# Kernel optimization log

Measured on AMD Instinct MI355X. Metric: run time of the kernel, lower is better.

## Reference

```python
import jax, jax.numpy as jnp
import numpy as np
import math

N, D = 4096, 1024


def setup_inputs() -> dict:
    key = jax.random.key(0)
    ks = jax.random.split(key, 8)
    vecs = jax.random.normal(ks[0], (N, D), dtype=jnp.float32)
    mass = jax.random.uniform(ks[1], (N,), dtype=jnp.float32)            # semantic mass in [0,1)
    hops = jax.random.uniform(ks[2], (N,), dtype=jnp.float32) * 5.0      # hop distances in [0,5)
    alive = jax.random.randint(ks[3], (N,), 0, 10) > 0
    is_photon = jax.random.randint(ks[4], (N,), 0, 10) == 0
    W_res_w = jax.random.normal(ks[5], (D, D), dtype=jnp.float32) / np.sqrt(D)
    W_res_b = jnp.zeros((D,), dtype=jnp.float32)
    w_conf_i = jax.random.normal(ks[6], (D,), dtype=jnp.float32) / np.sqrt(2 * D)
    w_conf_j = jax.random.normal(ks[7], (D,), dtype=jnp.float32) / np.sqrt(2 * D)
    b_conf = jnp.zeros((), dtype=jnp.float32)
    log_c = jnp.asarray(math.log(50.0), dtype=jnp.float32)  # 'relationship' domain
    log_G = jnp.zeros((), dtype=jnp.float32)
    return dict(vecs=vecs, mass=mass, hops=hops, alive=alive, is_photon=is_photon,
                W_res_w=W_res_w, W_res_b=W_res_b, w_conf_i=w_conf_i, w_conf_j=w_conf_j,
                b_conf=b_conf, log_c=log_c, log_G=log_G)


def reference(vecs, mass, hops, alive, is_photon, W_res_w, W_res_b,
              w_conf_i, w_conf_j, b_conf, log_c, log_G):
    n = vecs.shape[0]
    c = jnp.maximum(jnp.exp(log_c), 1e-6)
    G = jnp.exp(log_G)

    # Per-row quantities (phi() reads hops/photon from entity i).
    d_light = hops / c                                                   # [N]
    lam = jnp.where(is_photon, 1.0, jnp.exp(-d_light))                   # redshift, [N]
    r2 = jnp.maximum(d_light, 0.1) ** 2                                  # r_safe^2, [N]
    causal_decay = jnp.where(d_light <= 1.0, 1.0, jnp.exp(-d_light + 1.0))  # [N]

    # Causal mask: j must be strictly in the past (j < i).
    idx = jnp.arange(n)
    past = (idx[None, :] < idx[:, None]).astype(vecs.dtype)              # [N,N]
    C = past * causal_decay[:, None]

    # Gravity: G * m_i * m_j / r_i^2
    grav = G * (mass / r2)[:, None] * mass[None, :]                      # [N,N]

    # Resonance: cosine similarity of W_res projections (torch eps=1e-8 norm clamp).
    v = vecs @ W_res_w.T + W_res_b                                       # [N,D]
    vn = v / jnp.maximum(jnp.linalg.norm(v, axis=-1, keepdims=True), 1e-8)
    R = vn @ vn.T                                                        # [N,N]
    zero_norm = jnp.linalg.norm(vecs, axis=-1) < 1e-8                    # [N]
    R = jnp.where(zero_norm[:, None] | zero_norm[None, :], 0.0, R)

    # Conflict gate: sigmoid(W_conflict @ concat(v_i, v_j) + b) = sigmoid(s_i + s_j + b).
    s_i = vecs @ w_conf_i                                                # [N]
    s_j = vecs @ w_conf_j                                                # [N]
    conflict = jax.nn.sigmoid(s_i[:, None] + s_j[None, :] + b_conf)      # [N,N]

    phi_attract = lam[:, None] * grav * C * (0.5 + 0.5 * R)
    phi_repulse = -lam[:, None] * conflict * mass[:, None] * mass[None, :]
    phi = jnp.where(conflict > 0.8, phi_repulse, phi_attract)

    # Black holes and the diagonal produce zero field.
    gate = alive[:, None] & alive[None, :]
    phi = jnp.where(gate & (idx[:, None] != idx[None, :]), phi, 0.0)
    return phi
```

## Files before the change

### kernel.cpp

```cpp
#include <hip/hip_runtime.h>
#include <hip/hip_bf16.h>
#include <math.h>

#define NROW 4096
#define DIM  1024

typedef short v8s __attribute__((ext_vector_type(8)));
typedef float v4f __attribute__((ext_vector_type(4)));

__device__ __forceinline__ ushort f2bf(float f) {
    __hip_bfloat16 h = __float2bfloat16(f);
    union { __hip_bfloat16 h; ushort u; } x; x.h = h; return x.u;
}

__global__ __launch_bounds__(256) void k_rowstats(
    const float* __restrict__ vecs, const float* __restrict__ mass,
    const float* __restrict__ hops, const int* __restrict__ alive,
    const int* __restrict__ is_photon, const float* __restrict__ wci,
    const float* __restrict__ wcj, const float* __restrict__ logc,
    const float* __restrict__ logG, const float* __restrict__ bconf,
    double* __restrict__ s_i, double* __restrict__ s_j,
    float* __restrict__ rowAtt, float* __restrict__ rowRep,
    float* __restrict__ massF, int* __restrict__ flags)
{
    const int row = blockIdx.x, t = threadIdx.x;
    const float* vr = vecs + (size_t)row * DIM;
    const int base = t * 4;
    float4 pv = *(const float4*)&vr[base];
    float4 pi = *(const float4*)&wci[base];
    float4 pj = *(const float4*)&wcj[base];
    double di = (double)pv.x * pi.x + (double)pv.y * pi.y + (double)pv.z * pi.z + (double)pv.w * pi.w;
    double dj = (double)pv.x * pj.x + (double)pv.y * pj.y + (double)pv.z * pj.z + (double)pv.w * pj.w;
    double ss = (double)pv.x * pv.x + (double)pv.y * pv.y + (double)pv.z * pv.z + (double)pv.w * pv.w;
    #pragma unroll
    for (int off = 32; off > 0; off >>= 1) {
        di += __shfl_down(di, off);
        dj += __shfl_down(dj, off);
        ss += __shfl_down(ss, off);
    }
    __shared__ double rd[3][4];
    const int wid = t >> 6;
    if ((t & 63) == 0) { rd[0][wid] = di; rd[1][wid] = dj; rd[2][wid] = ss; }
    __syncthreads();
    if (t == 0) {
        di = rd[0][0] + rd[0][1] + rd[0][2] + rd[0][3];
        dj = rd[1][0] + rd[1][1] + rd[1][2] + rd[1][3];
        ss = rd[2][0] + rd[2][1] + rd[2][2] + rd[2][3];
        double c  = fmax(exp((double)logc[0]), 1e-6);
        double G  = exp((double)logG[0]);
        double dl = (double)hops[row] / c;
        double lam = (is_photon[row] != 0) ? 1.0 : exp(-dl);
        double rs  = fmax(dl, 0.1);
        double cd  = (dl <= 1.0) ? 1.0 : exp(-dl + 1.0);
        double m   = (double)mass[row];
        s_i[row] = di;
        s_j[row] = dj + (double)bconf[0];
        rowAtt[row] = (float)(lam * G * m / (rs * rs) * cd);
        rowRep[row] = (float)(-lam * m);
        massF[row]  = (float)m;
        flags[row]  = ((alive[row] != 0) ? 1 : 0) | ((sqrt(ss) < 1e-8) ? 2 : 0);
    }
}

__global__ __launch_bounds__(256) void k_proj(
    const float* __restrict__ A, const float* __restrict__ B,
    const float* __restrict__ bias, ushort* __restrict__ vout)
{
    __shared__ ushort As[128 * 32], Bs[128 * 32];
    const int t = threadIdx.x;
    const int m0 = blockIdx.y * 128, n0 = blockIdx.x * 128;
    const int wid = t >> 6, lane = t & 63;
    const int wm = wid >> 1, wn = wid & 1;
    const int quad = lane >> 4, l16 = lane & 15;
    v4f acc[4][4];
    #pragma unroll
    for (int i = 0; i < 4; i++)
        #pragma unroll
        for (int j = 0; j < 4; j++) acc[i][j] = (v4f){0.f, 0.f, 0.f, 0.f};

    for (int k0 = 0; k0 < DIM; k0 += 32) {
        #pragma unroll
        for (int p = 0; p < 4; ++p) {
            int c = p * 256 + t;
            int r = c >> 3, co = (c & 7) * 4;
            float4 fa = *(const float4*)&A[(size_t)(m0 + r) * DIM + k0 + co];
            float4 fb = *(const float4*)&B[(size_t)(n0 + r) * DIM + k0 + co];
            ushort4 ua, ub;
            ua.x = f2bf(fa.x); ua.y = f2bf(fa.y); ua.z = f2bf(fa.z); ua.w = f2bf(fa.w);
            ub.x = f2bf(fb.x); ub.y = f2bf(fb.y); ub.z = f2bf(fb.z); ub.w = f2bf(fb.w);
            *(ushort4*)&As[r * 32 + co] = ua;
            *(ushort4*)&Bs[r * 32 + co] = ub;
        }
        __syncthreads();
        v8s af[4], bfr[4];
        #pragma unroll
        for (int mi = 0; mi < 4; mi++) af[mi]  = *(const v8s*)&As[(wm * 64 + mi * 16 + l16) * 32 + quad * 8];
        #pragma unroll
        for (int ni = 0; ni < 4; ni++) bfr[ni] = *(const v8s*)&Bs[(wn * 64 + ni * 16 + l16) * 32 + quad * 8];
        #pragma unroll
        for (int mi = 0; mi < 4; mi++)
            #pragma unroll
            for (int ni = 0; ni < 4; ni++)
                acc[mi][ni] = __builtin_amdgcn_mfma_f32_16x16x32_bf16(af[mi], bfr[ni], acc[mi][ni], 0, 0, 0);
        __syncthreads();
    }
    float bcol[4];
    #pragma unroll
    for (int ni = 0; ni < 4; ni++) bcol[ni] = bias[n0 + wn * 64 + ni * 16 + l16];
    #pragma unroll
    for (int mi = 0; mi < 4; mi++)
        #pragma unroll
        for (int r = 0; r < 4; r++) {
            int row = m0 + wm * 64 + mi * 16 + quad * 4 + r;
            #pragma unroll
            for (int ni = 0; ni < 4; ni++) {
                int col = n0 + wn * 64 + ni * 16 + l16;
                vout[(size_t)row * DIM + col] = f2bf(acc[mi][ni][r] + bcol[ni]);
            }
        }
}

__global__ __launch_bounds__(256) void k_norm(ushort* __restrict__ v)
{
    const int row = blockIdx.x, t = threadIdx.x;
    ushort* vr = v + (size_t)row * DIM;
    ushort4 pv = *(const ushort4*)&vr[t * 4];
    union { unsigned i; float f; } c0, c1, c2, c3;
    c0.i = ((unsigned)pv.x) << 16; c1.i = ((unsigned)pv.y) << 16;
    c2.i = ((unsigned)pv.z) << 16; c3.i = ((unsigned)pv.w) << 16;
    float x0 = c0.f, x1 = c1.f, x2 = c2.f, x3 = c3.f;
    float ss = x0 * x0 + x1 * x1 + x2 * x2 + x3 * x3;
    #pragma unroll
    for (int off = 32; off > 0; off >>= 1) ss += __shfl_down(ss, off);
    __shared__ float r4[4];
    __shared__ float sinv;
    if ((t & 63) == 0) r4[t >> 6] = ss;
    __syncthreads();
    if (t == 0) sinv = 1.0f / fmaxf(sqrtf(r4[0] + r4[1] + r4[2] + r4[3]), 1e-8f);
    __syncthreads();
    float inv = sinv;
    ushort4 o;
    o.x = f2bf(x0 * inv); o.y = f2bf(x1 * inv); o.z = f2bf(x2 * inv); o.w = f2bf(x3 * inv);
    *(ushort4*)&vr[t * 4] = o;
}

__global__ __launch_bounds__(256) void k_phi(
    const ushort* __restrict__ vn,
    const double* __restrict__ s_i, const double* __restrict__ s_j,
    const float* __restrict__ rowAtt, const float* __restrict__ rowRep,
    const float* __restrict__ massF, const int* __restrict__ flags,
    float* __restrict__ out)
{
    __shared__ ushort As[128 * 32], Bs[128 * 32];
    const int t = threadIdx.x;
    const int id = blockIdx.x;
    const bool heavy = (id < 528);
    int bi, bj;
    if (heavy) {
        int r = 0;
        while (id >= ((r + 1) * (r + 2)) >> 1) ++r;
        bi = r; bj = id - ((r * (r + 1)) >> 1);
    } else {
        int l = id - 528;
        int r = 0;
        while (l >= 31 - r) { l -= 31 - r; ++r; }
        bi = r; bj = r + 1 + l;
    }
    const int m0 = bi * 128, n0 = bj * 128;
    const int wid = t >> 6, lane = t & 63;
    const int wm = wid >> 1, wn = wid & 1;
    const int quad = lane >> 4, l16 = lane & 15;

    const double LN4 = 1.3862943611198906;
    float  cm[4]; double csj[4]; int cf[4]; int ccol[4];
    #pragma unroll
    for (int ni = 0; ni < 4; ni++) {
        int col = n0 + wn * 64 + ni * 16 + l16;
        ccol[ni] = col; cm[ni] = massF[col]; csj[ni] = s_j[col]; cf[ni] = flags[col];
    }

    if (!heavy) {
        #pragma unroll
        for (int mi = 0; mi < 4; mi++)
            #pragma unroll
            for (int r = 0; r < 4; r++) {
                int row = m0 + wm * 64 + mi * 16 + quad * 4 + r;
                float  rR = rowRep[row];
                int    fi = flags[row];
                double si = s_i[row];
                size_t ob = (size_t)row * NROW;
                #pragma unroll
                for (int ni = 0; ni < 4; ni++) {
                    double x = si + csj[ni];
                    bool   hit = (x > LN4) && ((fi & cf[ni]) & 1);
                    float  conflict = 1.0f / (1.0f + expf(-(float)x));
                    out[ob + ccol[ni]] = hit ? rR * conflict * cm[ni] : 0.0f;
                }
            }
        return;
    }

    v4f acc[4][4];
    #pragma unroll
    for (int i = 0; i < 4; i++)
        #pragma unroll
        for (int j = 0; j < 4; j++) acc[i][j] = (v4f){0.f, 0.f, 0.f, 0.f};

    for (int k0 = 0; k0 < DIM; k0 += 32) {
        #pragma unroll
        for (int p = 0; p < 2; ++p) {
            int c = (wid * 2 + p) * 64 + lane;
            int r = c >> 2, co = (c & 3) * 8;
            const ushort* ga = &vn[(size_t)(m0 + r) * DIM + k0 + co];
            const ushort* gb = &vn[(size_t)(n0 + r) * DIM + k0 + co];
            __builtin_amdgcn_global_load_lds(
                (const __attribute__((address_space(1))) void*)ga,
                (__attribute__((address_space(3))) void*)&As[(wid * 2 + p) * 512], 16, 0, 0);
            __builtin_amdgcn_global_load_lds(
                (const __attribute__((address_space(1))) void*)gb,
                (__attribute__((address_space(3))) void*)&Bs[(wid * 2 + p) * 512], 16, 0, 0);
        }
        __syncthreads();
        v8s af[4], bfr[4];
        #pragma unroll
        for (int mi = 0; mi < 4; mi++) af[mi]  = *(const v8s*)&As[(wm * 64 + mi * 16 + l16) * 32 + quad * 8];
        #pragma unroll
        for (int ni = 0; ni < 4; ni++) bfr[ni] = *(const v8s*)&Bs[(wn * 64 + ni * 16 + l16) * 32 + quad * 8];
        #pragma unroll
        for (int mi = 0; mi < 4; mi++)
            #pragma unroll
            for (int ni = 0; ni < 4; ni++)
                acc[mi][ni] = __builtin_amdgcn_mfma_f32_16x16x32_bf16(af[mi], bfr[ni], acc[mi][ni], 0, 0, 0);
        __syncthreads();
    }

    #pragma unroll
    for (int mi = 0; mi < 4; mi++)
        #pragma unroll
        for (int r = 0; r < 4; r++) {
            int row = m0 + wm * 64 + mi * 16 + quad * 4 + r;
            float  rA = rowAtt[row], rR = rowRep[row];
            int    fi = flags[row];
            double si = s_i[row];
            size_t ob = (size_t)row * NROW;
            #pragma unroll
            for (int ni = 0; ni < 4; ni++) {
                int col = ccol[ni];
                double x = si + csj[ni];
                float conflict = 1.0f / (1.0f + expf(-(float)x));
                bool  chigh = x > LN4;
                bool  gate  = ((fi & cf[ni]) & 1) && (row != col);
                float Rv  = ((fi | cf[ni]) & 2) ? 0.0f : acc[mi][ni][r];
                float att = (col < row) ? rA * cm[ni] * (0.5f + 0.5f * Rv) : 0.0f;
                float ph  = gate ? (chigh ? rR * conflict * cm[ni] : att) : 0.0f;
                out[ob + col] = ph;
            }
        }
}

extern "C" void kernel_launch(void* const* d_in, const int* in_sizes, int n_in,
                              void* d_out, int out_size, void* d_ws, size_t ws_size,
                              hipStream_t stream)
{
    const float* vecs      = (const float*)d_in[0];
    const float* mass      = (const float*)d_in[1];
    const float* hops      = (const float*)d_in[2];
    const int*   alive     = (const int*)d_in[3];
    const int*   is_photon = (const int*)d_in[4];
    const float* W         = (const float*)d_in[5];
    const float* Wb        = (const float*)d_in[6];
    const float* wci       = (const float*)d_in[7];
    const float* wcj       = (const float*)d_in[8];
    const float* bconf     = (const float*)d_in[9];
    const float* logc      = (const float*)d_in[10];
    const float* logG      = (const float*)d_in[11];

    char* ws = (char*)d_ws;
    double* s_i    = (double*)(ws);
    double* s_j    = (double*)(ws + 32768);
    float*  rowAtt = (float*)(ws + 65536);
    float*  rowRep = (float*)(ws + 81920);
    float*  massF  = (float*)(ws + 98304);
    int*    flagsA = (int*)(ws + 114688);
    ushort* vn     = (ushort*)(ws + 131072);

    k_rowstats<<<dim3(NROW), dim3(256), 0, stream>>>(
        vecs, mass, hops, alive, is_photon, wci, wcj, logc, logG, bconf,
        s_i, s_j, rowAtt, rowRep, massF, flagsA);
    k_proj<<<dim3(DIM / 128, NROW / 128), dim3(256), 0, stream>>>(vecs, W, Wb, vn);
    k_norm<<<dim3(NROW), dim3(256), 0, stream>>>(vn);
    k_phi<<<dim3(1024), dim3(256), 0, stream>>>(
        vn, s_i, s_j, rowAtt, rowRep, massF, flagsA, (float*)d_out);
}
```

Measured before the change: 205.0 us.

## Fuse row normalization into projection GEMM and load MFMA operands directly from global

Removes the separate normalization kernel: the projection GEMM now accumulates squared row norms via atomics, and the phi kernel applies the inverse norms to the dot products in its epilogue. Both GEMMs drop the LDS staging and barriers, loading MFMA fragments straight from global memory with register double-buffering. Heavy and light tiles in the phi kernel are now interleaved across block IDs for better load balance. The cost is uncoalesced, non-shared global fragment loads that rely on cache reuse, plus atomic contention on the row-norm buffer.

```diff
diff --git a/kernel.cpp b/kernel.cpp
--- a/kernel.cpp
+++ b/kernel.cpp
@@ -11,6 +11,15 @@
 __device__ __forceinline__ ushort f2bf(float f) {
     __hip_bfloat16 h = __float2bfloat16(f);
     union { __hip_bfloat16 h; ushort u; } x; x.h = h; return x.u;
+}
+__device__ __forceinline__ v8s cvt8(const float* p) {
+    float4 a = *(const float4*)p, b = *(const float4*)(p + 4);
+    v8s r;
+    r[0] = (short)f2bf(a.x); r[1] = (short)f2bf(a.y);
+    r[2] = (short)f2bf(a.z); r[3] = (short)f2bf(a.w);
+    r[4] = (short)f2bf(b.x); r[5] = (short)f2bf(b.y);
+    r[6] = (short)f2bf(b.z); r[7] = (short)f2bf(b.w);
+    return r;
 }
 
 __global__ __launch_bounds__(256) void k_rowstats(
@@ -21,7 +30,8 @@
     const float* __restrict__ logG, const float* __restrict__ bconf,
     double* __restrict__ s_i, double* __restrict__ s_j,
     float* __restrict__ rowAtt, float* __restrict__ rowRep,
-    float* __restrict__ massF, int* __restrict__ flags)
+    float* __restrict__ massF, int* __restrict__ flags,
+    float* __restrict__ rownorm)
 {
     const int row = blockIdx.x, t = threadIdx.x;
     const float* vr = vecs + (size_t)row * DIM;
@@ -59,51 +69,61 @@
         rowRep[row] = (float)(-lam * m);
         massF[row]  = (float)m;
         flags[row]  = ((alive[row] != 0) ? 1 : 0) | ((sqrt(ss) < 1e-8) ? 2 : 0);
+        rownorm[row] = 0.0f;
     }
 }
 
 __global__ __launch_bounds__(256) void k_proj(
     const float* __restrict__ A, const float* __restrict__ B,
-    const float* __restrict__ bias, ushort* __restrict__ vout)
+    const float* __restrict__ bias, ushort* __restrict__ vout,
+    float* __restrict__ rownorm)
 {
-    __shared__ ushort As[128 * 32], Bs[128 * 32];
     const int t = threadIdx.x;
     const int m0 = blockIdx.y * 128, n0 = blockIdx.x * 128;
     const int wid = t >> 6, lane = t & 63;
     const int wm = wid >> 1, wn = wid & 1;
     const int quad = lane >> 4, l16 = lane & 15;
+
+    const float* pA[4]; const float* pB[4];
+    #pragma unroll
+    for (int mi = 0; mi < 4; mi++) pA[mi] = A + (size_t)(m0 + wm * 64 + mi * 16 + l16) * DIM + quad * 8;
+    #pragma unroll
+    for (int ni = 0; ni < 4; ni++) pB[ni] = B + (size_t)(n0 + wn * 64 + ni * 16 + l16) * DIM + quad * 8;
+
     v4f acc[4][4];
     #pragma unroll
     for (int i = 0; i < 4; i++)
         #pragma unroll
         for (int j = 0; j < 4; j++) acc[i][j] = (v4f){0.f, 0.f, 0.f, 0.f};
 
-    for (int k0 = 0; k0 < DIM; k0 += 32) {
-        #pragma unroll
-        for (int p = 0; p < 4; ++p) {
-            int c = p * 256 + t;
-            int r = c >> 3, co = (c & 7) * 4;
-            float4 fa = *(const float4*)&A[(size_t)(m0 + r) * DIM + k0 + co];
-            float4 fb = *(const float4*)&B[(size_t)(n0 + r) * DIM + k0 + co];
-            ushort4 ua, ub;
-            ua.x = f2bf(fa.x); ua.y = f2bf(fa.y); ua.z = f2bf(fa.z); ua.w = f2bf(fa.w);
-            ub.x = f2bf(fb.x); ub.y = f2bf(fb.y); ub.z = f2bf(fb.z); ub.w = f2bf(fb.w);
-            *(ushort4*)&As[r * 32 + co] = ua;
-            *(ushort4*)&Bs[r * 32 + co] = ub;
-        }
-        __syncthreads();
-        v8s af[4], bfr[4];
-        #pragma unroll
-        for (int mi = 0; mi < 4; mi++) af[mi]  = *(const v8s*)&As[(wm * 64 + mi * 16 + l16) * 32 + quad * 8];
-        #pragma unroll
-        for (int ni = 0; ni < 4; ni++) bfr[ni] = *(const v8s*)&Bs[(wn * 64 + ni * 16 + l16) * 32 + quad * 8];
+    v8s ca[4], cb[4];
+    #pragma unroll
+    for (int mi = 0; mi < 4; mi++) ca[mi] = cvt8(pA[mi]);
+    #pragma unroll
+    for (int ni = 0; ni < 4; ni++) cb[ni] = cvt8(pB[ni]);
+
+    for (int k = 32; k < DIM; k += 32) {
+        v8s na[4], nb[4];
+        #pragma unroll
+        for (int mi = 0; mi < 4; mi++) na[mi] = cvt8(pA[mi] + k);
+        #pragma unroll
+        for (int ni = 0; ni < 4; ni++) nb[ni] = cvt8(pB[ni] + k);
         #pragma unroll
         for (int mi = 0; mi < 4; mi++)
             #pragma unroll
             for (int ni = 0; ni < 4; ni++)
-                acc[mi][ni] = __builtin_amdgcn_mfma_f32_16x16x32_bf16(af[mi], bfr[ni], acc[mi][ni], 0, 0, 0);
-        __syncthreads();
-    }
+                acc[mi][ni] = __builtin_amdgcn_mfma_f32_16x16x32_bf16(ca[mi], cb[ni], acc[mi][ni], 0, 0, 0);
+        #pragma unroll
+        for (int mi = 0; mi < 4; mi++) ca[mi] = na[mi];
+        #pragma unroll
+        for (int ni = 0; ni < 4; ni++) cb[ni] = nb[ni];
+    }
+    #pragma unroll
+    for (int mi = 0; mi < 4; mi++)
+        #pragma unroll
+        for (int ni = 0; ni < 4; ni++)
+            acc[mi][ni] = __builtin_amdgcn_mfma_f32_16x16x32_bf16(ca[mi], cb[ni], acc[mi][ni], 0, 0, 0);
+
     float bcol[4];
     #pragma unroll
     for (int ni = 0; ni < 4; ni++) bcol[ni] = bias[n0 + wn * 64 + ni * 16 + l16];
@@ -112,36 +132,18 @@
         #pragma unroll
         for (int r = 0; r < 4; r++) {
             int row = m0 + wm * 64 + mi * 16 + quad * 4 + r;
+            float ss = 0.0f;
             #pragma unroll
             for (int ni = 0; ni < 4; ni++) {
                 int col = n0 + wn * 64 + ni * 16 + l16;
-                vout[(size_t)row * DIM + col] = f2bf(acc[mi][ni][r] + bcol[ni]);
+                float vv = acc[mi][ni][r] + bcol[ni];
+                vout[(size_t)row * DIM + col] = f2bf(vv);
+                ss += vv * vv;
             }
+            #pragma unroll
+            for (int off = 8; off > 0; off >>= 1) ss += __shfl_down(ss, off);
+            if (l16 == 0) atomicAdd(&rownorm[row], ss);
         }
-}
-
-__global__ __launch_bounds__(256) void k_norm(ushort* __restrict__ v)
-{
-    const int row = blockIdx.x, t = threadIdx.x;
-    ushort* vr = v + (size_t)row * DIM;
-    ushort4 pv = *(const ushort4*)&vr[t * 4];
-    union { unsigned i; float f; } c0, c1, c2, c3;
-    c0.i = ((unsigned)pv.x) << 16; c1.i = ((unsigned)pv.y) << 16;
-    c2.i = ((unsigned)pv.z) << 16; c3.i = ((unsigned)pv.w) << 16;
-    float x0 = c0.f, x1 = c1.f, x2 = c2.f, x3 = c3.f;
-    float ss = x0 * x0 + x1 * x1 + x2 * x2 + x3 * x3;
-    #pragma unroll
-    for (int off = 32; off > 0; off >>= 1) ss += __shfl_down(ss, off);
-    __shared__ float r4[4];
-    __shared__ float sinv;
-    if ((t & 63) == 0) r4[t >> 6] = ss;
-    __syncthreads();
-    if (t == 0) sinv = 1.0f / fmaxf(sqrtf(r4[0] + r4[1] + r4[2] + r4[3]), 1e-8f);
-    __syncthreads();
-    float inv = sinv;
-    ushort4 o;
-    o.x = f2bf(x0 * inv); o.y = f2bf(x1 * inv); o.z = f2bf(x2 * inv); o.w = f2bf(x3 * inv);
-    *(ushort4*)&vr[t * 4] = o;
 }
 
 __global__ __launch_bounds__(256) void k_phi(
@@ -149,19 +151,20 @@
     const double* __restrict__ s_i, const double* __restrict__ s_j,
     const float* __restrict__ rowAtt, const float* __restrict__ rowRep,
     const float* __restrict__ massF, const int* __restrict__ flags,
-    float* __restrict__ out)
+    const float* __restrict__ rownorm, float* __restrict__ out)
 {
-    __shared__ ushort As[128 * 32], Bs[128 * 32];
     const int t = threadIdx.x;
     const int id = blockIdx.x;
-    const bool heavy = (id < 528);
+    const int h  = (id * 528) >> 10;
+    const int h2 = ((id + 1) * 528) >> 10;
+    const bool heavy = (h2 > h);
     int bi, bj;
     if (heavy) {
         int r = 0;
-        while (id >= ((r + 1) * (r + 2)) >> 1) ++r;
-        bi = r; bj = id - ((r * (r + 1)) >> 1);
+        while (h >= ((r + 1) * (r + 2)) >> 1) ++r;
+        bi = r; bj = h - ((r * (r + 1)) >> 1);
     } else {
-        int l = id - 528;
+        int l = id - h;
         int r = 0;
         while (l >= 31 - r) { l -= 31 - r; ++r; }
         bi = r; bj = r + 1 + l;
@@ -200,39 +203,50 @@
         return;
     }
 
+    const ushort* pA[4]; const ushort* pB[4];
+    #pragma unroll
+    for (int mi = 0; mi < 4; mi++) pA[mi] = vn + (size_t)(m0 + wm * 64 + mi * 16 + l16) * DIM + quad * 8;
+    #pragma unroll
+    for (int ni = 0; ni < 4; ni++) pB[ni] = vn + (size_t)(n0 + wn * 64 + ni * 16 + l16) * DIM + quad * 8;
+
     v4f acc[4][4];
     #pragma unroll
     for (int i = 0; i < 4; i++)
         #pragma unroll
         for (int j = 0; j < 4; j++) acc[i][j] = (v4f){0.f, 0.f, 0.f, 0.f};
 
-    for (int k0 = 0; k0 < DIM; k0 += 32) {
-        #pragma unroll
-        for (int p = 0; p < 2; ++p) {
-            int c = (wid * 2 + p) * 64 + lane;
-            int r = c >> 2, co = (c & 3) * 8;
-            const ushort* ga = &vn[(size_t)(m0 + r) * DIM + k0 + co];
-            const ushort* gb = &vn[(size_t)(n0 + r) * DIM + k0 + co];
-            __builtin_amdgcn_global_load_lds(
-                (const __attribute__((address_space(1))) void*)ga,
-                (__attribute__((address_space(3))) void*)&As[(wid * 2 + p) * 512], 16, 0, 0);
-            __builtin_amdgcn_global_load_lds(
-                (const __attribute__((address_space(1))) void*)gb,
-                (__attribute__((address_space(3))) void*)&Bs[(wid * 2 + p) * 512], 16, 0, 0);
-        }
-        __syncthreads();
-        v8s af[4], bfr[4];
-        #pragma unroll
-        for (int mi = 0; mi < 4; mi++) af[mi]  = *(const v8s*)&As[(wm * 64 + mi * 16 + l16) * 32 + quad * 8];
-        #pragma unroll
-        for (int ni = 0; ni < 4; ni++) bfr[ni] = *(const v8s*)&Bs[(wn * 64 + ni * 16 + l16) * 32 + quad * 8];
+    v8s ca[4], cb[4];
+    #pragma unroll
+    for (int mi = 0; mi < 4; mi++) ca[mi] = *(const v8s*)pA[mi];
+    #pragma unroll
+    for (int ni = 0; ni < 4; ni++) cb[ni] = *(const v8s*)pB[ni];
+
+    for (int k = 32; k < DIM; k += 32) {
+        v8s na[4], nb[4];
+        #pragma unroll
+        for (int mi = 0; mi < 4; mi++) na[mi] = *(const v8s*)(pA[mi] + k);
+        #pragma unroll
+        for (int ni = 0; ni < 4; ni++) nb[ni] = *(const v8s*)(pB[ni] + k);
         #pragma unroll
         for (int mi = 0; mi < 4; mi++)
             #pragma unroll
             for (int ni = 0; ni < 4; ni++)
-                acc[mi][ni] = __builtin_amdgcn_mfma_f32_16x16x32_bf16(af[mi], bfr[ni], acc[mi][ni], 0, 0, 0);
-        __syncthreads();
-    }
+                acc[mi][ni] = __builtin_amdgcn_mfma_f32_16x16x32_bf16(ca[mi], cb[ni], acc[mi][ni], 0, 0, 0);
+        #pragma unroll
+        for (int mi = 0; mi < 4; mi++) ca[mi] = na[mi];
+        #pragma unroll
+        for (int ni = 0; ni < 4; ni++) cb[ni] = nb[ni];
+    }
+    #pragma unroll
+    for (int mi = 0; mi < 4; mi++)
+        #pragma unroll
+        for (int ni = 0; ni < 4; ni++)
+            acc[mi][ni] = __builtin_amdgcn_mfma_f32_16x16x32_bf16(ca[mi], cb[ni], acc[mi][ni], 0, 0, 0);
+
+    float cinv[4];
+    #pragma unroll
+    for (int ni = 0; ni < 4; ni++)
+        cinv[ni] = 1.0f / fmaxf(sqrtf(rownorm[ccol[ni]]), 1e-8f);
 
     #pragma unroll
     for (int mi = 0; mi < 4; mi++)
@@ -240,6 +254,7 @@
         for (int r = 0; r < 4; r++) {
             int row = m0 + wm * 64 + mi * 16 + quad * 4 + r;
             float  rA = rowAtt[row], rR = rowRep[row];
+            float  riv = 1.0f / fmaxf(sqrtf(rownorm[row]), 1e-8f);
             int    fi = flags[row];
             double si = s_i[row];
             size_t ob = (size_t)row * NROW;
@@ -250,7 +265,7 @@
                 float conflict = 1.0f / (1.0f + expf(-(float)x));
                 bool  chigh = x > LN4;
                 bool  gate  = ((fi & cf[ni]) & 1) && (row != col);
-                float Rv  = ((fi | cf[ni]) & 2) ? 0.0f : acc[mi][ni][r];
+                float Rv  = ((fi | cf[ni]) & 2) ? 0.0f : acc[mi][ni][r] * riv * cinv[ni];
                 float att = (col < row) ? rA * cm[ni] * (0.5f + 0.5f * Rv) : 0.0f;
                 float ph  = gate ? (chigh ? rR * conflict * cm[ni] : att) : 0.0f;
                 out[ob + col] = ph;
@@ -276,19 +291,19 @@
     const float* logG      = (const float*)d_in[11];
 
     char* ws = (char*)d_ws;
-    double* s_i    = (double*)(ws);
-    double* s_j    = (double*)(ws + 32768);
-    float*  rowAtt = (float*)(ws + 65536);
-    float*  rowRep = (float*)(ws + 81920);
-    float*  massF  = (float*)(ws + 98304);
-    int*    flagsA = (int*)(ws + 114688);
-    ushort* vn     = (ushort*)(ws + 131072);
+    double* s_i     = (double*)(ws);
+    double* s_j     = (double*)(ws + 32768);
+    float*  rowAtt  = (float*)(ws + 65536);
+    float*  rowRep  = (float*)(ws + 81920);
+    float*  massF   = (float*)(ws + 98304);
+    int*    flagsA  = (int*)(ws + 114688);
+    float*  rownorm = (float*)(ws + 131072);
+    ushort* vn      = (ushort*)(ws + 147456);
 
     k_rowstats<<<dim3(NROW), dim3(256), 0, stream>>>(
         vecs, mass, hops, alive, is_photon, wci, wcj, logc, logG, bconf,
-        s_i, s_j, rowAtt, rowRep, massF, flagsA);
-    k_proj<<<dim3(DIM / 128, NROW / 128), dim3(256), 0, stream>>>(vecs, W, Wb, vn);
-    k_norm<<<dim3(NROW), dim3(256), 0, stream>>>(vn);
+        s_i, s_j, rowAtt, rowRep, massF, flagsA, rownorm);
+    k_proj<<<dim3(DIM / 128, NROW / 128), dim3(256), 0, stream>>>(vecs, W, Wb, vn, rownorm);
     k_phi<<<dim3(1024), dim3(256), 0, stream>>>(
-        vn, s_i, s_j, rowAtt, rowRep, massF, flagsA, (float*)d_out);
-}
+        vn, s_i, s_j, rowAtt, rowRep, massF, flagsA, rownorm, (float*)d_out);
+}
```

Result: slower. 291.6 us (+42.3%).
